# Optimization experiments

Hardware: AMD Instinct MI355X
Metric: run time of the kernel (lower is better)

The kernel has to match this reference:

```python
import jax, jax.numpy as jnp
import numpy as np

B, L, N, F, H, ED, HOR = 64, 24, 512, 2, 128, 16, 12


def setup_inputs() -> dict:
    key = jax.random.key(0)
    ks = jax.random.split(key, 9)
    g = lambda k, shp, sc: jax.random.normal(k, shp, dtype=jnp.float32) * sc
    return {
        "X": g(ks[0], (B, L, N, F), 1.0),
        "E": g(ks[1], (N, ED), 1.0),
        "W1": g(ks[2], (ED, ED), ED ** -0.5),
        "W2": g(ks[3], (ED, ED), ED ** -0.5),
        "Wz": g(ks[4], (F + H, H), (F + H) ** -0.5),
        "bz": jnp.zeros((H,), jnp.float32),
        "Wr": g(ks[5], (F + H, H), (F + H) ** -0.5),
        "br": jnp.zeros((H,), jnp.float32),
        "Wh": g(ks[6], (F + H, H), (F + H) ** -0.5),
        "bh": jnp.zeros((H,), jnp.float32),
        "Whead": g(ks[7], (H, HOR), H ** -0.5),
        "bhead": jnp.zeros((HOR,), jnp.float32),
    }


def reference(X, E, W1, W2, Wz, bz, Wr, br, Wh, bh, Whead, bhead):
    # Adaptive adjacency: A = softmax(relu((E W1)(E W2)^T))  -> [N, N]
    M1 = E @ W1
    M2 = E @ W2
    A = jax.nn.softmax(jax.nn.relu(M1 @ M2.T), axis=-1)

    b, n, h = X.shape[0], X.shape[2], Wz.shape[1]

    def step(hprev, x_t):  # x_t: [B, N, F], hprev: [B, N, H]
        inp = jnp.concatenate([x_t, hprev], axis=-1)          # [B, N, F+H]
        g = jnp.einsum('nm,bmf->bnf', A, inp)                  # graph conv mix
        z = jax.nn.sigmoid(g @ Wz + bz)
        r = jax.nn.sigmoid(g @ Wr + br)
        inp_r = jnp.concatenate([x_t, r * hprev], axis=-1)
        gh = jnp.einsum('nm,bmf->bnf', A, inp_r)
        h_tilde = jnp.tanh(gh @ Wh + bh)
        hnew = (1.0 - z) * hprev + z * h_tilde
        return hnew, None

    h0 = jnp.zeros((b, n, h), X.dtype)
    h_final, _ = jax.lax.scan(step, h0, jnp.moveaxis(X, 1, 0))  # scan over L
    out = h_final @ Whead + bhead                                # [B, N, HOR]
    return jnp.transpose(out, (0, 2, 1))                         # [B, HOR, N]
```

## Files before the change

### kernel.cpp

```cpp
#include <hip/hip_runtime.h>

typedef _Float16 f16;
typedef _Float16 f16x8 __attribute__((ext_vector_type(8)));
typedef float f32x4 __attribute__((ext_vector_type(4)));

typedef const __attribute__((address_space(1))) void GV;
typedef __attribute__((address_space(3))) void LV;

__device__ __forceinline__ void gload16(const void* g, void* l) {
  __builtin_amdgcn_global_load_lds((GV*)g, (LV*)l, 16, 0, 0);
}

#define WAIT_VM0() asm volatile("s_waitcnt vmcnt(0)" ::: "memory")

__device__ __forceinline__ f16x8 ntload16(const f16* p) {
  f16x8 v;
  asm volatile("global_load_dwordx4 %0, %1, off sc0 sc1" : "=v"(v) : "v"(p) : "memory");
  return v;
}
__device__ __forceinline__ void ntstore16(f16* p, f16x8 v) {
  asm volatile("global_store_dwordx4 %0, %1, off sc0 sc1" :: "v"(p), "v"(v) : "memory");
}

__device__ __forceinline__ void group_sync(unsigned* bar, unsigned target) {
  __syncthreads();
  if (threadIdx.x == 0) {
    atomicAdd(bar, 1u);
    int guard = 0;
    while (1) {
      unsigned v;
      asm volatile("global_load_dword %0, %1, off sc0 sc1\n\ts_waitcnt vmcnt(0)"
                   : "=v"(v) : "v"(bar) : "memory");
      if (v >= target || ++guard > (1 << 22)) break;
      __builtin_amdgcn_s_sleep(8);
    }
  }
  __syncthreads();
}

__device__ __forceinline__ f16x8 frag64(const f16* T, int row, int chunk) {
  int ch = chunk ^ (row & 7);
  return *(const f16x8*)((const char*)T + row * 128 + ch * 16);
}
__device__ __forceinline__ f16x8 frag128(const f16* T, int row, int chunk) {
  int ch = chunk ^ (row & 15);
  return *(const f16x8*)((const char*)T + row * 256 + ch * 16);
}
__device__ __forceinline__ f16* elem128(f16* T, int row, int col) {
  return (f16*)((char*)T + row * 256 + (((col >> 3) ^ (row & 15)) << 4) + (col & 7) * 2);
}

#define MFMA(a, b, c) __builtin_amdgcn_mfma_f32_16x16x32_f16(a, b, c, 0, 0, 0)

__device__ __forceinline__ float sigm(float v) {
  return __builtin_amdgcn_rcpf(1.f + __expf(-v));
}
__device__ __forceinline__ float tanh_(float v) {
  return 1.f - 2.f * __builtin_amdgcn_rcpf(1.f + __expf(2.f * v));
}

__device__ __forceinline__ void issue64(const f16* Ab, const f16* Bb, int k0,
                                        char* bufA, f16x8 (&c)[4],
                                        const size_t (&offs)[4], int wb) {
#pragma unroll
  for (int q = 0; q < 4; ++q)
    gload16(Ab + k0 + offs[q], bufA + q * 4096 + wb);
#pragma unroll
  for (int q = 0; q < 4; ++q)
    c[q] = ntload16(Bb + k0 + offs[q]);
}
__device__ __forceinline__ void wr64(char* bufB, const f16x8 (&c)[4], int tb) {
#pragma unroll
  for (int q = 0; q < 4; ++q)
    *(f16x8*)(bufB + q * 4096 + tb) = c[q];
}
__device__ __forceinline__ void comp64(const char* buf, int wm, int wn, int g, int r,
                                       f32x4 (&acc)[4][4]) {
  const f16* Ta = (const f16*)buf;
  const f16* Tb = (const f16*)(buf + 16384);
#pragma unroll
  for (int kk = 0; kk < 2; ++kk) {
    f16x8 af[4], bf[4];
#pragma unroll
    for (int i = 0; i < 4; ++i) af[i] = frag64(Ta, wm + i * 16 + r, (kk << 2) | g);
#pragma unroll
    for (int j = 0; j < 4; ++j) bf[j] = frag64(Tb, wn + j * 16 + r, (kk << 2) | g);
#pragma unroll
    for (int i = 0; i < 4; ++i)
#pragma unroll
      for (int j = 0; j < 4; ++j)
        acc[i][j] = MFMA(af[i], bf[j], acc[i][j]);
  }
}

__device__ __forceinline__ void phase1(const f16* At, const f16* Bb, char* sm,
    const size_t (&offs)[4], int wm, int wn, int g, int r, f32x4 (&acc)[4][4]) {
  const int tid = threadIdx.x;
  const int wb = (tid >> 6) * 1024;
  const int tb = tid * 16;
  f16x8 c[4];
  issue64(At, Bb, 0, sm, c, offs, wb);
  WAIT_VM0();
  wr64(sm + 16384, c, tb);
  __syncthreads();
#pragma unroll 1
  for (int kt = 0; kt < 8; ++kt) {
    char* cur = sm + (kt & 1) * 32768;
    char* nxt = sm + ((kt & 1) ^ 1) * 32768;
    if (kt < 7) issue64(At, Bb, (kt + 1) * 64, nxt, c, offs, wb);
    comp64(cur, wm, wn, g, r, acc);
    if (kt < 7) { WAIT_VM0(); wr64(nxt + 16384, c, tb); }
    __syncthreads();
  }
}

__device__ __forceinline__ void gate_gemm(const f16* Gs, const f16* WT,
                                          int wm, int wn, int g, int r,
                                          f32x4 (&acc)[4][4]) {
#pragma unroll
  for (int kk = 0; kk < 4; ++kk) {
    f16x8 wf[4], af[4];
#pragma unroll
    for (int j = 0; j < 4; ++j)
      wf[j] = *(const f16x8*)&WT[(size_t)(wn + j * 16 + r) * 128 + kk * 32 + g * 8];
#pragma unroll
    for (int i = 0; i < 4; ++i) af[i] = frag128(Gs, wm + i * 16 + r, (kk << 2) | g);
#pragma unroll
    for (int i = 0; i < 4; ++i)
#pragma unroll
      for (int j = 0; j < 4; ++j)
        acc[i][j] = MFMA(af[i], wf[j], acc[i][j]);
  }
}

__global__ __launch_bounds__(256, 1)
void persist(const f16* __restrict__ A16, const f16* __restrict__ AX,
             const f16* __restrict__ WzT, const f16* __restrict__ WrT,
             const f16* __restrict__ WhT,
             const float* __restrict__ Wzf, const float* __restrict__ bz,
             const float* __restrict__ Wrf, const float* __restrict__ br,
             const float* __restrict__ Whf, const float* __restrict__ bh,
             const float* __restrict__ Whead, const float* __restrict__ bhead,
             f16* __restrict__ Ha, f16* __restrict__ Hb,
             f16* __restrict__ RH, unsigned* __restrict__ bar,
             float* __restrict__ out) {
  __shared__ __align__(16) char sm[70656];
  f16* Gs = (f16*)(sm + 32768);
  f16* Ct = (f16*)(sm + 0);
  f16* AXs = (f16*)(sm + 65536);
  float* wp = (float*)(sm + 66048);

  const int tid = threadIdx.x;
  const int lane = tid & 63;
  const int g = lane >> 4, r = lane & 15;
  const int wid = tid >> 6;
  const int wm = (wid >> 1) * 64, wn = (wid & 1) * 64;
  const int b = blockIdx.x >> 2, nc = blockIdx.x & 3;
  const int m0 = nc * 128;

  for (int idx = tid; idx < 1152; idx += 256) {
    int row = idx >> 7, j = idx & 127;
    float v;
    if (row == 0) v = Wzf[j];
    else if (row == 1) v = Wzf[128 + j];
    else if (row == 2) v = bz[j];
    else if (row == 3) v = Wrf[j];
    else if (row == 4) v = Wrf[128 + j];
    else if (row == 5) v = br[j];
    else if (row == 6) v = Whf[j];
    else if (row == 7) v = Whf[128 + j];
    else v = bh[j];
    wp[idx] = v;
  }

  size_t offs[4];
#pragma unroll
  for (int q = 0; q < 4; ++q) {
    int lin = q * 4096 + tid * 16;
    int row = lin >> 7;
    int ch = ((lin >> 4) & 7) ^ (row & 7);
    offs[q] = (size_t)row * 512 + ch * 8;
  }

  const f16* Atile = A16 + (size_t)m0 * 512;
  const size_t boff = (size_t)b * 65536;
  f16* rh = RH + boff;
  unsigned* mybar = bar + b * 16;
  unsigned nbar = 0;
  f16x8 zreg[8];
  f16x8 hvreg[8] = {};
  __syncthreads();

#pragma unroll 1
  for (int t = 0; t < 24; ++t) {
    const f16* hc = ((t & 1) ? Hb : Ha) + boff;
    f16* hn = ((t & 1) ? Ha : Hb) + boff;
    if (tid < 128) {
      int cf = b * 48 + t * 2;
      const f16* p = AX + (size_t)(cf >> 7) * 65536 + (size_t)(m0 + tid) * 128 + (cf & 127);
      AXs[2 * tid] = p[0];
      AXs[2 * tid + 1] = p[1];
    }
    f32x4 acc[4][4] = {};
    phase1(Atile, hc, sm, offs, wm, wn, g, r, acc);
#pragma unroll
    for (int i = 0; i < 4; ++i)
#pragma unroll
      for (int j = 0; j < 4; ++j)
#pragma unroll
        for (int q = 0; q < 4; ++q)
          *elem128(Gs, wm + i * 16 + g * 4 + q, wn + j * 16 + r) = (f16)acc[i][j][q];
    __syncthreads();
    {
      f32x4 az[4][4] = {};
      gate_gemm(Gs, WzT, wm, wn, g, r, az);
#pragma unroll
      for (int i = 0; i < 4; ++i)
#pragma unroll
        for (int j = 0; j < 4; ++j)
#pragma unroll
          for (int q = 0; q < 4; ++q)
            *elem128(Ct, wn + j * 16 + r, wm + i * 16 + g * 4 + q) = (f16)az[i][j][q];
      __syncthreads();
#pragma unroll
      for (int p = 0; p < 8; ++p) {
        int hh = p * 16 + (tid >> 4), c = tid & 15, nl0 = c * 8;
        f16x8 cv = frag128(Ct, hh, c);
        float w0 = wp[hh], w1 = wp[128 + hh], bb = wp[256 + hh];
        f16x8 o;
#pragma unroll
        for (int u = 0; u < 8; ++u) {
          int nl = nl0 + u;
          float gx = (float)AXs[2 * nl] * w0 + (float)AXs[2 * nl + 1] * w1 + bb;
          o[u] = (f16)sigm((float)cv[u] + gx);
        }
        zreg[p] = o;
      }
      __syncthreads();
    }
    {
      f32x4 ar[4][4] = {};
      gate_gemm(Gs, WrT, wm, wn, g, r, ar);
#pragma unroll
      for (int i = 0; i < 4; ++i)
#pragma unroll
        for (int j = 0; j < 4; ++j)
#pragma unroll
          for (int q = 0; q < 4; ++q)
            *elem128(Ct, wn + j * 16 + r, wm + i * 16 + g * 4 + q) = (f16)ar[i][j][q];
      __syncthreads();
#pragma unroll
      for (int p = 0; p < 8; ++p) {
        int hh = p * 16 + (tid >> 4), c = tid & 15, nl0 = c * 8;
        f16x8 cv = frag128(Ct, hh, c);
        f16x8 hv = hvreg[p];
        float w0 = wp[384 + hh], w1 = wp[512 + hh], bb = wp[640 + hh];
        f16x8 o;
#pragma unroll
        for (int u = 0; u < 8; ++u) {
          int nl = nl0 + u;
          float gx = (float)AXs[2 * nl] * w0 + (float)AXs[2 * nl + 1] * w1 + bb;
          float rv = sigm((float)cv[u] + gx);
          o[u] = (f16)(rv * (float)hv[u]);
        }
        ntstore16(&rh[(size_t)hh * 512 + m0 + nl0], o);
      }
      WAIT_VM0();
    }
    group_sync(mybar, 4u * (++nbar));
    f32x4 acc2[4][4] = {};
    phase1(Atile, rh, sm, offs, wm, wn, g, r, acc2);
#pragma unroll
    for (int i = 0; i < 4; ++i)
#pragma unroll
      for (int j = 0; j < 4; ++j)
#pragma unroll
        for (int q = 0; q < 4; ++q)
          *elem128(Gs, wm + i * 16 + g * 4 + q, wn + j * 16 + r) = (f16)acc2[i][j][q];
    __syncthreads();
    {
      f32x4 ah[4][4] = {};
      gate_gemm(Gs, WhT, wm, wn, g, r, ah);
#pragma unroll
      for (int i = 0; i < 4; ++i)
#pragma unroll
        for (int j = 0; j < 4; ++j)
#pragma unroll
          for (int q = 0; q < 4; ++q)
            *elem128(Ct, wn + j * 16 + r, wm + i * 16 + g * 4 + q) = (f16)ah[i][j][q];
      __syncthreads();
#pragma unroll
      for (int p = 0; p < 8; ++p) {
        int hh = p * 16 + (tid >> 4), c = tid & 15, nl0 = c * 8;
        f16x8 cv = frag128(Ct, hh, c);
        float w0 = wp[768 + hh], w1 = wp[896 + hh], bb = wp[1024 + hh];
        f16x8 hv = hvreg[p], zv = zreg[p];
        f16x8 o;
#pragma unroll
        for (int u = 0; u < 8; ++u) {
          int nl = nl0 + u;
          float gx = (float)AXs[2 * nl] * w0 + (float)AXs[2 * nl + 1] * w1 + bb;
          float ht = tanh_((float)cv[u] + gx);
          float z = (float)zv[u];
          o[u] = (f16)((1.f - z) * (float)hv[u] + z * ht);
        }
        hvreg[p] = o;
        if (t < 23) {
          ntstore16(&hn[(size_t)hh * 512 + m0 + nl0], o);
        } else {
          *(f16x8*)((char*)Gs + hh * 256 + nl0 * 2) = o;
        }
      }
      if (t < 23) WAIT_VM0();
    }
    if (t < 23) {
      group_sync(mybar, 4u * (++nbar));
    }
  }

  __syncthreads();
  float* Ws = (float*)Ct;
  for (int idx = tid; idx < 1548; idx += 256)
    Ws[idx] = (idx < 1536) ? Whead[idx] : bhead[idx - 1536];
  __syncthreads();
  {
    int n = tid & 127, hf = tid >> 7;
    float pa[12];
#pragma unroll
    for (int o = 0; o < 12; ++o) pa[o] = 0.f;
    const f16* Hfin = (const f16*)Gs;
    for (int h = hf * 64; h < hf * 64 + 64; ++h) {
      float v = (float)Hfin[h * 128 + n];
#pragma unroll
      for (int o = 0; o < 12; ++o) pa[o] = fmaf(v, Ws[h * 12 + o], pa[o]);
    }
    float* P = (float*)(sm + 16384);
#pragma unroll
    for (int o = 0; o < 12; ++o) P[(n * 2 + hf) * 12 + o] = pa[o];
    __syncthreads();
    if (hf == 0) {
#pragma unroll
      for (int o = 0; o < 12; ++o)
        out[(size_t)b * 6144 + o * 512 + m0 + n] =
            P[n * 24 + o] + P[n * 24 + 12 + o] + Ws[1536 + o];
    }
  }
}

__device__ __forceinline__ void stage128x64(const f16* src, int row0, int ld, int k0,
                                            f16* lds, int tid) {
  int wid = tid >> 6;
#pragma unroll
  for (int q = 0; q < 4; ++q) {
    int lin = q * 4096 + tid * 16;
    int row = lin >> 7;
    int ch = (lin >> 4) & 7;
    int sch = ch ^ (row & 7);
    gload16(src + (size_t)(row0 + row) * ld + k0 + sch * 8,
            (char*)lds + q * 4096 + wid * 1024);
  }
}

__global__ __launch_bounds__(256, 2)
void gemm512(const f16* __restrict__ A, const f16* __restrict__ B,
             f16* __restrict__ C) {
  __shared__ __align__(16) char sm[34816];
  f16* As = (f16*)sm;
  f16* Bs = (f16*)(sm + 16384);
  const int tid = threadIdx.x;
  const int lane = tid & 63;
  const int g = lane >> 4, r = lane & 15;
  const int wid = tid >> 6;
  const int wm = (wid >> 1) * 64, wn = (wid & 1) * 64;
  const int m0 = blockIdx.y * 128;
  const int n0 = blockIdx.x * 128;
  f32x4 acc[4][4] = {};
  for (int kt = 0; kt < 8; ++kt) {
    stage128x64(A, m0, 512, kt * 64, As, tid);
    stage128x64(B, n0, 512, kt * 64, Bs, tid);
    __syncthreads();
#pragma unroll
    for (int kk = 0; kk < 2; ++kk) {
      f16x8 af[4], bf[4];
#pragma unroll
      for (int i = 0; i < 4; ++i) af[i] = frag64(As, wm + i * 16 + r, (kk << 2) | g);
#pragma unroll
      for (int j = 0; j < 4; ++j) bf[j] = frag64(Bs, wn + j * 16 + r, (kk << 2) | g);
#pragma unroll
      for (int i = 0; i < 4; ++i)
#pragma unroll
        for (int j = 0; j < 4; ++j)
          acc[i][j] = MFMA(af[i], bf[j], acc[i][j]);
    }
    __syncthreads();
  }
  f16* Ctl = (f16*)sm;
#pragma unroll
  for (int i = 0; i < 4; ++i)
#pragma unroll
    for (int j = 0; j < 4; ++j) {
      int col = wn + j * 16 + r;
#pragma unroll
      for (int q = 0; q < 4; ++q) {
        int row = wm + i * 16 + g * 4 + q;
        Ctl[row * 136 + col] = (f16)acc[i][j][q];
      }
    }
  __syncthreads();
  f16* Cb = C + (size_t)blockIdx.x * 65536;
#pragma unroll
  for (int p = 0; p < 8; ++p) {
    int row = p * 16 + (tid >> 4);
    int c0 = (tid & 15) * 8;
    f16x8 v = *(const f16x8*)&Ctl[row * 136 + c0];
    *(f16x8*)&Cb[(size_t)(m0 + row) * 128 + c0] = v;
  }
}

__global__ void m12k(const float* __restrict__ E, const float* __restrict__ W1,
                     const float* __restrict__ W2, float* __restrict__ M1,
                     float* __restrict__ M2) {
  int idx = blockIdx.x * 256 + threadIdx.x;
  if (idx >= 16384) return;
  int which = idx >> 13;
  int rem = idx & 8191;
  int n = rem >> 4, j = rem & 15;
  const float* W = which ? W2 : W1;
  float s = 0.f;
#pragma unroll
  for (int k = 0; k < 16; ++k) s += E[n * 16 + k] * W[k * 16 + j];
  (which ? M2 : M1)[n * 16 + j] = s;
}

__global__ __launch_bounds__(256)
void softA(const float* __restrict__ M1, const float* __restrict__ M2,
           f16* __restrict__ A16) {
  __shared__ float M2s[8192];
  __shared__ float m1s[16];
  __shared__ float red[8];
  int i = blockIdx.x, tid = threadIdx.x;
  for (int q = tid; q < 8192; q += 256) M2s[q] = M2[q];
  if (tid < 16) m1s[tid] = M1[i * 16 + tid];
  __syncthreads();
  float s0 = 0.f, s1 = 0.f;
#pragma unroll
  for (int k = 0; k < 16; ++k) {
    float a = m1s[k];
    s0 += a * M2s[tid * 16 + k];
    s1 += a * M2s[(tid + 256) * 16 + k];
  }
  s0 = fmaxf(s0, 0.f);
  s1 = fmaxf(s1, 0.f);
  float m = fmaxf(s0, s1);
  for (int o = 32; o > 0; o >>= 1) m = fmaxf(m, __shfl_xor(m, o));
  if ((tid & 63) == 0) red[tid >> 6] = m;
  __syncthreads();
  m = fmaxf(fmaxf(red[0], red[1]), fmaxf(red[2], red[3]));
  float e0 = expf(s0 - m), e1 = expf(s1 - m);
  float ss = e0 + e1;
  for (int o = 32; o > 0; o >>= 1) ss += __shfl_xor(ss, o);
  __syncthreads();
  if ((tid & 63) == 0) red[4 + (tid >> 6)] = ss;
  __syncthreads();
  ss = (red[4] + red[5]) + (red[6] + red[7]);
  float inv = 1.f / ss;
  A16[(size_t)i * 512 + tid] = (f16)(e0 * inv);
  A16[(size_t)i * 512 + tid + 256] = (f16)(e1 * inv);
}

__global__ void wTk(const float* __restrict__ Wz, const float* __restrict__ Wr,
                    const float* __restrict__ Wh, f16* __restrict__ WzT,
                    f16* __restrict__ WrT, f16* __restrict__ WhT) {
  int idx = blockIdx.x * 256 + threadIdx.x;
  if (idx >= 49152) return;
  int w = idx / 16384;
  int rem = idx & 16383;
  int hp = rem >> 7, k = rem & 127;
  const float* S = (w == 0) ? Wz : ((w == 1) ? Wr : Wh);
  f16* D = (w == 0) ? WzT : ((w == 1) ? WrT : WhT);
  D[hp * 128 + k] = (f16)S[(2 + k) * 128 + hp];
}

__global__ void xTk(const float* __restrict__ X, f16* __restrict__ XTT) {
  int idx = blockIdx.x * 256 + threadIdx.x;
  if (idx >= 786432) return;
  int m = idx & 511;
  int bt = idx >> 9;
  float x0 = X[(size_t)idx * 2];
  float x1 = X[(size_t)idx * 2 + 1];
  XTT[(size_t)(bt * 2 + 0) * 512 + m] = (f16)x0;
  XTT[(size_t)(bt * 2 + 1) * 512 + m] = (f16)x1;
}

extern "C" void kernel_launch(void* const* d_in, const int* in_sizes, int n_in,
                              void* d_out, int out_size, void* d_ws, size_t ws_size,
                              hipStream_t stream) {
  (void)in_sizes; (void)n_in; (void)out_size; (void)ws_size;
  const float* X = (const float*)d_in[0];
  const float* E = (const float*)d_in[1];
  const float* W1 = (const float*)d_in[2];
  const float* W2 = (const float*)d_in[3];
  const float* Wz = (const float*)d_in[4];
  const float* bz = (const float*)d_in[5];
  const float* Wr = (const float*)d_in[6];
  const float* br = (const float*)d_in[7];
  const float* Wh = (const float*)d_in[8];
  const float* bh = (const float*)d_in[9];
  const float* Whead = (const float*)d_in[10];
  const float* bhead = (const float*)d_in[11];
  float* out = (float*)d_out;
  char* ws = (char*)d_ws;

  f16* A16 = (f16*)(ws + 0);
  f16* XTT = (f16*)(ws + 524288);
  f16* AX  = (f16*)(ws + 3670016);
  f16* Ha  = (f16*)(ws + 6815744);
  f16* Hb  = (f16*)(ws + 15204352);
  f16* RH  = (f16*)(ws + 23592960);
  f16* WzT = (f16*)(ws + 31981568);
  f16* WrT = (f16*)(ws + 32014336);
  f16* WhT = (f16*)(ws + 32047104);
  float* M1 = (float*)(ws + 32079872);
  float* M2 = (float*)(ws + 32112640);
  unsigned* bar = (unsigned*)(ws + 32145408);

  hipMemsetAsync(Ha, 0, 8388608, stream);
  hipMemsetAsync(bar, 0, 16384, stream);
  m12k<<<64, 256, 0, stream>>>(E, W1, W2, M1, M2);
  softA<<<512, 256, 0, stream>>>(M1, M2, A16);
  wTk<<<192, 256, 0, stream>>>(Wz, Wr, Wh, WzT, WrT, WhT);
  xTk<<<3072, 256, 0, stream>>>(X, XTT);
  gemm512<<<dim3(24, 4), 256, 0, stream>>>(A16, XTT, AX);
  persist<<<256, 256, 0, stream>>>(A16, AX, WzT, WrT, WhT, Wz, bz, Wr, br, Wh, bh,
                                   Whead, bhead, Ha, Hb, RH, bar, out);
}
```

Before: 813.3 us.

## Use 512 threads per persistent block with 64x32 wave tiles

Doubles the persistent GRU kernel's block size from 4 to 8 waves. The 128x128 output tile is now split into 64x32 per-wave tiles, so the staging loads, MFMA loops, gate epilogues and head reduction are all re-indexed for 512 threads. The aim is more waves per CU to hide global-load and LDS latency on the serial recurrence, and less accumulator register pressure per wave. In exchange, each wave reloads A fragments for half as many outputs, which raises LDS read traffic, and synchronisation now covers more waves.

```diff
diff --git a/kernel.cpp b/kernel.cpp
--- a/kernel.cpp
+++ b/kernel.cpp
@@ -60,46 +60,46 @@
 }
 
 __device__ __forceinline__ void issue64(const f16* Ab, const f16* Bb, int k0,
-                                        char* bufA, f16x8 (&c)[4],
-                                        const size_t (&offs)[4], int wb) {
-#pragma unroll
-  for (int q = 0; q < 4; ++q)
-    gload16(Ab + k0 + offs[q], bufA + q * 4096 + wb);
-#pragma unroll
-  for (int q = 0; q < 4; ++q)
+                                        char* bufA, f16x8 (&c)[2],
+                                        const size_t (&offs)[2], int wid) {
+#pragma unroll
+  for (int q = 0; q < 2; ++q)
+    gload16(Ab + k0 + offs[q], bufA + q * 8192 + wid * 1024);
+#pragma unroll
+  for (int q = 0; q < 2; ++q)
     c[q] = ntload16(Bb + k0 + offs[q]);
 }
-__device__ __forceinline__ void wr64(char* bufB, const f16x8 (&c)[4], int tb) {
-#pragma unroll
-  for (int q = 0; q < 4; ++q)
-    *(f16x8*)(bufB + q * 4096 + tb) = c[q];
+__device__ __forceinline__ void wr64(char* bufB, const f16x8 (&c)[2], int tb) {
+#pragma unroll
+  for (int q = 0; q < 2; ++q)
+    *(f16x8*)(bufB + q * 8192 + tb) = c[q];
 }
 __device__ __forceinline__ void comp64(const char* buf, int wm, int wn, int g, int r,
-                                       f32x4 (&acc)[4][4]) {
+                                       f32x4 (&acc)[4][2]) {
   const f16* Ta = (const f16*)buf;
   const f16* Tb = (const f16*)(buf + 16384);
 #pragma unroll
   for (int kk = 0; kk < 2; ++kk) {
-    f16x8 af[4], bf[4];
+    f16x8 af[4], bf[2];
 #pragma unroll
     for (int i = 0; i < 4; ++i) af[i] = frag64(Ta, wm + i * 16 + r, (kk << 2) | g);
 #pragma unroll
-    for (int j = 0; j < 4; ++j) bf[j] = frag64(Tb, wn + j * 16 + r, (kk << 2) | g);
+    for (int j = 0; j < 2; ++j) bf[j] = frag64(Tb, wn + j * 16 + r, (kk << 2) | g);
 #pragma unroll
     for (int i = 0; i < 4; ++i)
 #pragma unroll
-      for (int j = 0; j < 4; ++j)
+      for (int j = 0; j < 2; ++j)
         acc[i][j] = MFMA(af[i], bf[j], acc[i][j]);
   }
 }
 
 __device__ __forceinline__ void phase1(const f16* At, const f16* Bb, char* sm,
-    const size_t (&offs)[4], int wm, int wn, int g, int r, f32x4 (&acc)[4][4]) {
+    const size_t (&offs)[2], int wid, int wm, int wn, int g, int r,
+    f32x4 (&acc)[4][2]) {
   const int tid = threadIdx.x;
-  const int wb = (tid >> 6) * 1024;
   const int tb = tid * 16;
-  f16x8 c[4];
-  issue64(At, Bb, 0, sm, c, offs, wb);
+  f16x8 c[2];
+  issue64(At, Bb, 0, sm, c, offs, wid);
   WAIT_VM0();
   wr64(sm + 16384, c, tb);
   __syncthreads();
@@ -107,7 +107,7 @@
   for (int kt = 0; kt < 8; ++kt) {
     char* cur = sm + (kt & 1) * 32768;
     char* nxt = sm + ((kt & 1) ^ 1) * 32768;
-    if (kt < 7) issue64(At, Bb, (kt + 1) * 64, nxt, c, offs, wb);
+    if (kt < 7) issue64(At, Bb, (kt + 1) * 64, nxt, c, offs, wid);
     comp64(cur, wm, wn, g, r, acc);
     if (kt < 7) { WAIT_VM0(); wr64(nxt + 16384, c, tb); }
     __syncthreads();
@@ -116,24 +116,24 @@
 
 __device__ __forceinline__ void gate_gemm(const f16* Gs, const f16* WT,
                                           int wm, int wn, int g, int r,
-                                          f32x4 (&acc)[4][4]) {
+                                          f32x4 (&acc)[4][2]) {
 #pragma unroll
   for (int kk = 0; kk < 4; ++kk) {
-    f16x8 wf[4], af[4];
-#pragma unroll
-    for (int j = 0; j < 4; ++j)
+    f16x8 wf[2], af[4];
+#pragma unroll
+    for (int j = 0; j < 2; ++j)
       wf[j] = *(const f16x8*)&WT[(size_t)(wn + j * 16 + r) * 128 + kk * 32 + g * 8];
 #pragma unroll
     for (int i = 0; i < 4; ++i) af[i] = frag128(Gs, wm + i * 16 + r, (kk << 2) | g);
 #pragma unroll
     for (int i = 0; i < 4; ++i)
 #pragma unroll
-      for (int j = 0; j < 4; ++j)
+      for (int j = 0; j < 2; ++j)
         acc[i][j] = MFMA(af[i], wf[j], acc[i][j]);
   }
 }
 
-__global__ __launch_bounds__(256, 1)
+__global__ __launch_bounds__(512, 1)
 void persist(const f16* __restrict__ A16, const f16* __restrict__ AX,
              const f16* __restrict__ WzT, const f16* __restrict__ WrT,
              const f16* __restrict__ WhT,
@@ -154,11 +154,12 @@
   const int lane = tid & 63;
   const int g = lane >> 4, r = lane & 15;
   const int wid = tid >> 6;
-  const int wm = (wid >> 1) * 64, wn = (wid & 1) * 64;
+  const int wm = (wid >> 2) * 64;
+  const int wn = (wid & 3) * 32;
   const int b = blockIdx.x >> 2, nc = blockIdx.x & 3;
   const int m0 = nc * 128;
 
-  for (int idx = tid; idx < 1152; idx += 256) {
+  for (int idx = tid; idx < 1152; idx += 512) {
     int row = idx >> 7, j = idx & 127;
     float v;
     if (row == 0) v = Wzf[j];
@@ -173,10 +174,10 @@
     wp[idx] = v;
   }
 
-  size_t offs[4];
-#pragma unroll
-  for (int q = 0; q < 4; ++q) {
-    int lin = q * 4096 + tid * 16;
+  size_t offs[2];
+#pragma unroll
+  for (int q = 0; q < 2; ++q) {
+    int lin = q * 8192 + tid * 16;
     int row = lin >> 7;
     int ch = ((lin >> 4) & 7) ^ (row & 7);
     offs[q] = (size_t)row * 512 + ch * 8;
@@ -187,8 +188,8 @@
   f16* rh = RH + boff;
   unsigned* mybar = bar + b * 16;
   unsigned nbar = 0;
-  f16x8 zreg[8];
-  f16x8 hvreg[8] = {};
+  f16x8 zreg[4];
+  f16x8 hvreg[4] = {};
   __syncthreads();
 
 #pragma unroll 1
@@ -201,30 +202,30 @@
       AXs[2 * tid] = p[0];
       AXs[2 * tid + 1] = p[1];
     }
-    f32x4 acc[4][4] = {};
-    phase1(Atile, hc, sm, offs, wm, wn, g, r, acc);
+    f32x4 acc[4][2] = {};
+    phase1(Atile, hc, sm, offs, wid, wm, wn, g, r, acc);
 #pragma unroll
     for (int i = 0; i < 4; ++i)
 #pragma unroll
-      for (int j = 0; j < 4; ++j)
+      for (int j = 0; j < 2; ++j)
 #pragma unroll
         for (int q = 0; q < 4; ++q)
           *elem128(Gs, wm + i * 16 + g * 4 + q, wn + j * 16 + r) = (f16)acc[i][j][q];
     __syncthreads();
     {
-      f32x4 az[4][4] = {};
+      f32x4 az[4][2] = {};
       gate_gemm(Gs, WzT, wm, wn, g, r, az);
 #pragma unroll
       for (int i = 0; i < 4; ++i)
 #pragma unroll
-        for (int j = 0; j < 4; ++j)
+        for (int j = 0; j < 2; ++j)
 #pragma unroll
           for (int q = 0; q < 4; ++q)
             *elem128(Ct, wn + j * 16 + r, wm + i * 16 + g * 4 + q) = (f16)az[i][j][q];
       __syncthreads();
 #pragma unroll
-      for (int p = 0; p < 8; ++p) {
-        int hh = p * 16 + (tid >> 4), c = tid & 15, nl0 = c * 8;
+      for (int p = 0; p < 4; ++p) {
+        int hh = p * 32 + (tid >> 4), c = tid & 15, nl0 = c * 8;
         f16x8 cv = frag128(Ct, hh, c);
         float w0 = wp[hh], w1 = wp[128 + hh], bb = wp[256 + hh];
         f16x8 o;
@@ -239,19 +240,19 @@
       __syncthreads();
     }
     {
-      f32x4 ar[4][4] = {};
+      f32x4 ar[4][2] = {};
       gate_gemm(Gs, WrT, wm, wn, g, r, ar);
 #pragma unroll
       for (int i = 0; i < 4; ++i)
 #pragma unroll
-        for (int j = 0; j < 4; ++j)
+        for (int j = 0; j < 2; ++j)
 #pragma unroll
           for (int q = 0; q < 4; ++q)
             *elem128(Ct, wn + j * 16 + r, wm + i * 16 + g * 4 + q) = (f16)ar[i][j][q];
       __syncthreads();
 #pragma unroll
-      for (int p = 0; p < 8; ++p) {
-        int hh = p * 16 + (tid >> 4), c = tid & 15, nl0 = c * 8;
+      for (int p = 0; p < 4; ++p) {
+        int hh = p * 32 + (tid >> 4), c = tid & 15, nl0 = c * 8;
         f16x8 cv = frag128(Ct, hh, c);
         f16x8 hv = hvreg[p];
         float w0 = wp[384 + hh], w1 = wp[512 + hh], bb = wp[640 + hh];
@@ -268,30 +269,30 @@
       WAIT_VM0();
     }
     group_sync(mybar, 4u * (++nbar));
-    f32x4 acc2[4][4] = {};
-    phase1(Atile, rh, sm, offs, wm, wn, g, r, acc2);
+    f32x4 acc2[4][2] = {};
+    phase1(Atile, rh, sm, offs, wid, wm, wn, g, r, acc2);
 #pragma unroll
     for (int i = 0; i < 4; ++i)
 #pragma unroll
-      for (int j = 0; j < 4; ++j)
+      for (int j = 0; j < 2; ++j)
 #pragma unroll
         for (int q = 0; q < 4; ++q)
           *elem128(Gs, wm + i * 16 + g * 4 + q, wn + j * 16 + r) = (f16)acc2[i][j][q];
     __syncthreads();
     {
-      f32x4 ah[4][4] = {};
+      f32x4 ah[4][2] = {};
       gate_gemm(Gs, WhT, wm, wn, g, r, ah);
 #pragma unroll
       for (int i = 0; i < 4; ++i)
 #pragma unroll
-        for (int j = 0; j < 4; ++j)
+        for (int j = 0; j < 2; ++j)
 #pragma unroll
           for (int q = 0; q < 4; ++q)
             *elem128(Ct, wn + j * 16 + r, wm + i * 16 + g * 4 + q) = (f16)ah[i][j][q];
       __syncthreads();
 #pragma unroll
-      for (int p = 0; p < 8; ++p) {
-        int hh = p * 16 + (tid >> 4), c = tid & 15, nl0 = c * 8;
+      for (int p = 0; p < 4; ++p) {
+        int hh = p * 32 + (tid >> 4), c = tid & 15, nl0 = c * 8;
         f16x8 cv = frag128(Ct, hh, c);
         float w0 = wp[768 + hh], w1 = wp[896 + hh], bb = wp[1024 + hh];
         f16x8 hv = hvreg[p], zv = zreg[p];
@@ -320,29 +321,30 @@
 
   __syncthreads();
   float* Ws = (float*)Ct;
-  for (int idx = tid; idx < 1548; idx += 256)
+  for (int idx = tid; idx < 1548; idx += 512)
     Ws[idx] = (idx < 1536) ? Whead[idx] : bhead[idx - 1536];
   __syncthreads();
   {
-    int n = tid & 127, hf = tid >> 7;
+    int n = tid & 127, qt = tid >> 7;
     float pa[12];
 #pragma unroll
     for (int o = 0; o < 12; ++o) pa[o] = 0.f;
     const f16* Hfin = (const f16*)Gs;
-    for (int h = hf * 64; h < hf * 64 + 64; ++h) {
+    for (int h = qt * 32; h < qt * 32 + 32; ++h) {
       float v = (float)Hfin[h * 128 + n];
 #pragma unroll
       for (int o = 0; o < 12; ++o) pa[o] = fmaf(v, Ws[h * 12 + o], pa[o]);
     }
-    float* P = (float*)(sm + 16384);
-#pragma unroll
-    for (int o = 0; o < 12; ++o) P[(n * 2 + hf) * 12 + o] = pa[o];
+    float* P = (float*)(sm + 8192);
+#pragma unroll
+    for (int o = 0; o < 12; ++o) P[(n * 4 + qt) * 12 + o] = pa[o];
     __syncthreads();
-    if (hf == 0) {
+    if (qt == 0) {
 #pragma unroll
       for (int o = 0; o < 12; ++o)
         out[(size_t)b * 6144 + o * 512 + m0 + n] =
-            P[n * 24 + o] + P[n * 24 + 12 + o] + Ws[1536 + o];
+            (P[n * 48 + o] + P[n * 48 + 12 + o]) +
+            (P[n * 48 + 24 + o] + P[n * 48 + 36 + o]) + Ws[1536 + o];
     }
   }
 }
@@ -531,6 +533,6 @@
   wTk<<<192, 256, 0, stream>>>(Wz, Wr, Wh, WzT, WrT, WhT);
   xTk<<<3072, 256, 0, stream>>>(X, XTT);
   gemm512<<<dim3(24, 4), 256, 0, stream>>>(A16, XTT, AX);
-  persist<<<256, 256, 0, stream>>>(A16, AX, WzT, WrT, WhT, Wz, bz, Wr, br, Wh, bh,
+  persist<<<256, 512, 0, stream>>>(A16, AX, WzT, WrT, WhT, Wz, bz, Wr, br, Wh, bh,
                                    Whead, bhead, Ha, Hb, RH, bar, out);
 }
```

Result: faster. 716.4 us (-11.9%).
